# Optimization experiments

Hardware: AMD Instinct MI355X
Metric: run time of the kernel (lower is better)

## Reference

```python
import jax, jax.numpy as jnp
import numpy as np

B, S, E = 2, 2048, 2048
H, KV, D = 16, 4, 128


def setup_inputs() -> dict:
    key = jax.random.key(0)
    k0, k1, k2, k3, k4 = jax.random.split(key, 5)
    s = 0.02  # init scale for weights
    return {
        "x": jax.random.normal(k0, (B, S, E), jnp.float32),
        "wq": jax.random.normal(k1, (E, H * D), jnp.float32) * s,
        "wk": jax.random.normal(k2, (E, KV * D), jnp.float32) * s,
        "wv": jax.random.normal(k3, (E, KV * D), jnp.float32) * s,
        "wo": jax.random.normal(k4, (H * D, E), jnp.float32) * s,
    }


def _rope_tables(seq_len, head_dim, dtype):
    inv_freq = 1.0 / (10000.0 ** (jnp.arange(0, head_dim, 2, dtype=jnp.float32) / head_dim))
    t = jnp.arange(seq_len, dtype=jnp.float32)
    freqs = jnp.outer(t, inv_freq)  # [S, D/2]
    emb = jnp.concatenate([freqs, freqs], axis=-1)  # [S, D]
    cos = jnp.cos(emb).astype(dtype)[None, None]  # [1,1,S,D]
    sin = jnp.sin(emb).astype(dtype)[None, None]
    return cos, sin


def _rotate_half(x):
    x1, x2 = jnp.split(x, 2, axis=-1)
    return jnp.concatenate([-x2, x1], axis=-1)


def reference(x, wq, wk, wv, wo):
    b, s, _ = x.shape
    # projections -> [B, heads, S, D]
    q = (x @ wq).reshape(b, s, H, D).transpose(0, 2, 1, 3)
    k = (x @ wk).reshape(b, s, KV, D).transpose(0, 2, 1, 3)
    v = (x @ wv).reshape(b, s, KV, D).transpose(0, 2, 1, 3)
    # inline RoPE (rotate-half convention), applied to q and k
    cos, sin = _rope_tables(s, D, q.dtype)
    q = q * cos + _rotate_half(q) * sin
    k = k * cos + _rotate_half(k) * sin
    # GQA: duplicate K/V heads (repeat_interleave along head dim)
    rep = H // KV
    k = jnp.repeat(k, rep, axis=1)
    v = jnp.repeat(v, rep, axis=1)
    scale = 1.0 / np.sqrt(D)
    scores = jnp.einsum('bhqd,bhkd->bhqk', q, k) * scale  # [B,H,S,S]
    attn = jax.nn.softmax(scores.astype(jnp.float32), axis=-1).astype(q.dtype)
    out = jnp.einsum('bhqk,bhkd->bhqd', attn, v)  # [B,H,S,D]
    out = out.transpose(0, 2, 1, 3).reshape(b, s, H * D)
    return out @ wo
```

## Files before the change

kernel.cpp:

```cpp
#include <hip/hip_runtime.h>
#include <hip/hip_bf16.h>

typedef __attribute__((ext_vector_type(8))) short s16x8;
typedef __attribute__((ext_vector_type(4))) float f32x4;
typedef __attribute__((ext_vector_type(16))) float f32x16;

__device__ inline float bf2f(unsigned short u) {
  union { unsigned int i; float f; } v; v.i = ((unsigned int)u) << 16; return v.f;
}
__device__ inline unsigned short f2bf(float f) {
  union { float f; unsigned int i; } v; v.f = f;
  unsigned int r = (v.i + 0x7FFFu + ((v.i >> 16) & 1u)) >> 16;
  return (unsigned short)r;
}
__device__ inline void gl_lds16(const void* g, void* l) {
  __builtin_amdgcn_global_load_lds(
      (const __attribute__((address_space(1))) unsigned int*)g,
      (__attribute__((address_space(3))) unsigned int*)l, 16, 0, 0);
}

__global__ __launch_bounds__(256) void cast_to_bf16(const float* __restrict__ s,
                                                    unsigned short* __restrict__ d, int n4) {
  int i = blockIdx.x * 256 + threadIdx.x;
  if (i >= n4) return;
  float4 v = ((const float4*)s)[i];
  ushort4 o;
  o.x = f2bf(v.x); o.y = f2bf(v.y); o.z = f2bf(v.z); o.w = f2bf(v.w);
  ((ushort4*)d)[i] = o;
}

__global__ __launch_bounds__(256) void transpose_cast(const float* __restrict__ src,
                                                      unsigned short* __restrict__ dst,
                                                      int K, int N) {
  __shared__ float tile[32][33];
  int n0 = blockIdx.x * 32, k0 = blockIdx.y * 32;
  int tx = threadIdx.x & 31, ty = threadIdx.x >> 5;
#pragma unroll
  for (int i = 0; i < 4; ++i) {
    int k = ty + i * 8;
    tile[k][tx] = src[(size_t)(k0 + k) * N + n0 + tx];
  }
  __syncthreads();
#pragma unroll
  for (int i = 0; i < 4; ++i) {
    int n = ty + i * 8;
    dst[(size_t)(n0 + n) * K + k0 + tx] = f2bf(tile[tx][n]);
  }
}

__global__ __launch_bounds__(256) void rope_tables(float* __restrict__ ct, float* __restrict__ st) {
  int idx = blockIdx.x * 256 + threadIdx.x;
  int s = idx >> 6, i = idx & 63;
  float inv = powf(10000.0f, -(float)(2 * i) * (1.0f / 128.0f));
  float ang = (float)s * inv;
  ct[idx] = cosf(ang);
  st[idx] = sinf(ang);
}

__global__ __launch_bounds__(256) void rope_apply(unsigned short* __restrict__ qkv,
                                                  const float* __restrict__ ct,
                                                  const float* __restrict__ st) {
  int row = blockIdx.x;
  int pos = row & 2047;
  unsigned short* base = qkv + (size_t)row * 3072;
  for (int it = threadIdx.x; it < 1280; it += 256) {
    int head = it >> 6, dh = it & 63;
    int col = head < 16 ? head * 128 : 2048 + (head - 16) * 128;
    float a = bf2f(base[col + dh]);
    float b = bf2f(base[col + dh + 64]);
    float c = ct[pos * 64 + dh], sn = st[pos * 64 + dh];
    base[col + dh] = f2bf(a * c - b * sn);
    base[col + dh + 64] = f2bf(b * c + a * sn);
  }
}

__global__ __launch_bounds__(256) void vtrans(const unsigned short* __restrict__ qkv,
                                              unsigned short* __restrict__ vt) {
  __shared__ unsigned short tile[32][33];
  int tx = threadIdx.x & 31, ty = threadIdx.x >> 5;
  int s0 = blockIdx.x * 32;
  int d0 = blockIdx.y * 32;
  int bz = blockIdx.z;
  const unsigned short* src = qkv + (size_t)((bz >> 2) * 2048) * 3072 + 2560 + (bz & 3) * 128;
#pragma unroll
  for (int i = 0; i < 4; ++i)
    tile[ty + i * 8][tx] = src[(size_t)(s0 + ty + i * 8) * 3072 + d0 + tx];
  __syncthreads();
  unsigned short* dst = vt + (size_t)bz * 128 * 2048;
#pragma unroll
  for (int i = 0; i < 4; ++i)
    dst[(size_t)(d0 + ty + i * 8) * 2048 + s0 + tx] = tile[tx][ty + i * 8];
}

template <int BF16OUT>
__global__ __launch_bounds__(512, 2) void gemm256(const unsigned short* __restrict__ A,
                                                  const unsigned short* __restrict__ BT,
                                                  void* __restrict__ Cv,
                                                  int M, int N, int K) {
  __shared__ __align__(16) unsigned short Lds[2][4][256 * 32];
  const int t = threadIdx.x, lane = t & 63;
  const int wid = t >> 6, m16 = lane & 15, l4 = lane >> 4;
  const int wm = wid >> 2, wn = wid & 3;
  const int swA = (l4 ^ ((m16 >> 1) & 3)) * 16;

  int gx = gridDim.x, nwg = gx * gridDim.y;
  int wg = blockIdx.y * gx + blockIdx.x;
  if ((nwg & 7) == 0) { int q = nwg >> 3; wg = (wg & 7) * q + (wg >> 3); }
  const int rowBase = (wg / gx) * 256, colBase = (wg % gx) * 256;

  const int r0 = t >> 2, c80 = (t & 3) ^ ((r0 >> 1) & 3);
  const int g1 = 512 + t, r1 = g1 >> 2, c81 = (g1 & 3) ^ ((r1 >> 1) & 3);
  const char* pA0 = (const char*)(A + (size_t)(rowBase + r0) * K + c80 * 8);
  const char* pA1 = (const char*)(A + (size_t)(rowBase + r1) * K + c81 * 8);
  const char* pB0 = (const char*)(BT + (size_t)(colBase + r0) * K + c80 * 8);
  const char* pB1 = (const char*)(BT + (size_t)(colBase + r1) * K + c81 * 8);

  f32x4 acc[8][4];
#pragma unroll
  for (int fr = 0; fr < 8; ++fr)
#pragma unroll
    for (int fn = 0; fn < 4; ++fn) {
      f32x4 z = {0.f, 0.f, 0.f, 0.f};
      acc[fr][fn] = z;
    }
  s16x8 bf[4];

#define STG(mat, kc, kt, buf)                                             \
  {                                                                       \
    size_t ko = (size_t)((kt) * 64 + (kc) * 32) * 2;                      \
    char* pl = (char*)&Lds[buf][(mat) * 2 + (kc)][0];                     \
    gl_lds16(((mat) ? pB0 : pA0) + ko, pl + t * 16);                      \
    gl_lds16(((mat) ? pB1 : pA1) + ko, pl + 8192 + t * 16);               \
  }

#define GATE()                                         \
  asm volatile("s_waitcnt vmcnt(8)" ::: "memory");     \
  __builtin_amdgcn_s_barrier();                        \
  __builtin_amdgcn_sched_barrier(0);

#define CMP(cur, kc, frh)                                                          \
  {                                                                                \
    const char* Ap = (const char*)&Lds[cur][kc][0];                                \
    s16x8 af[4];                                                                   \
    _Pragma("unroll") for (int i = 0; i < 4; ++i)                                  \
        af[i] = *(const s16x8*)(Ap + (wm * 128 + ((frh) * 4 + i) * 16 + m16) * 64 + swA); \
    if ((frh) == 0) {                                                              \
      const char* Bp = (const char*)&Lds[cur][2 + (kc)][0];                        \
      _Pragma("unroll") for (int n = 0; n < 4; ++n)                                \
          bf[n] = *(const s16x8*)(Bp + (wn * 64 + n * 16 + m16) * 64 + swA);       \
    }                                                                              \
    __builtin_amdgcn_s_setprio(1);                                                 \
    _Pragma("unroll") for (int i = 0; i < 4; ++i)                                  \
        _Pragma("unroll") for (int n = 0; n < 4; ++n)                              \
            acc[(frh) * 4 + i][n] = __builtin_amdgcn_mfma_f32_16x16x32_bf16(       \
                af[i], bf[n], acc[(frh) * 4 + i][n], 0, 0, 0);                     \
    __builtin_amdgcn_s_setprio(0);                                                 \
  }

  const int NT = K >> 6;
  STG(0, 0, 0, 0); STG(1, 0, 0, 0);
  STG(0, 1, 0, 0); STG(1, 1, 0, 0);
  STG(0, 0, 1, 1); STG(1, 0, 1, 1);

  for (int kt = 0; kt < NT; ++kt) {
    const int cur = kt & 1;
    GATE();
    if (kt + 1 < NT) STG(0, 1, kt + 1, cur ^ 1);
    CMP(cur, 0, 0);
    __builtin_amdgcn_s_barrier();
    if (kt + 1 < NT) STG(1, 1, kt + 1, cur ^ 1);
    CMP(cur, 0, 1);
    GATE();
    if (kt + 2 < NT) STG(0, 0, kt + 2, cur);
    CMP(cur, 1, 0);
    __builtin_amdgcn_s_barrier();
    if (kt + 2 < NT) STG(1, 0, kt + 2, cur);
    CMP(cur, 1, 1);
  }
#undef STG
#undef GATE
#undef CMP

#pragma unroll
  for (int fr = 0; fr < 8; ++fr)
#pragma unroll
    for (int fn = 0; fn < 4; ++fn) {
      int rr = rowBase + wm * 128 + fr * 16 + l4 * 4;
      int cc = colBase + wn * 64 + fn * 16 + m16;
#pragma unroll
      for (int jr = 0; jr < 4; ++jr) {
        if (BF16OUT)
          ((unsigned short*)Cv)[(size_t)(rr + jr) * N + cc] = f2bf(acc[fr][fn][jr]);
        else
          ((float*)Cv)[(size_t)(rr + jr) * N + cc] = acc[fr][fn][jr];
      }
    }
}

__global__ __launch_bounds__(512, 2) void gemm256_n128(const unsigned short* __restrict__ A,
                                                       const unsigned short* __restrict__ BT,
                                                       float* __restrict__ Cv,
                                                       int M, int N, int K) {
  __shared__ __align__(16) char Lds[98304];
  const int t = threadIdx.x, lane = t & 63;
  const int wid = t >> 6, m16 = lane & 15, l4 = lane >> 4;
  const int wm = wid >> 2, wn = wid & 3;
  const int swA = (l4 ^ ((m16 >> 1) & 3)) * 16;

  int gx = gridDim.x, nwg = gx * gridDim.y;
  int wg = blockIdx.y * gx + blockIdx.x;
  if ((nwg & 7) == 0) { int q = nwg >> 3; wg = (wg & 7) * q + (wg >> 3); }
  const int rowBase = (wg / gx) * 256, colBase = (wg % gx) * 128;

  const int r0 = t >> 2, c80 = (t & 3) ^ ((r0 >> 1) & 3);
  const int g1 = 512 + t, r1 = g1 >> 2, c81 = (g1 & 3) ^ ((r1 >> 1) & 3);
  const char* pA0 = (const char*)(A + (size_t)(rowBase + r0) * K + c80 * 8);
  const char* pA1 = (const char*)(A + (size_t)(rowBase + r1) * K + c81 * 8);
  const char* pB0 = (const char*)(BT + (size_t)(colBase + r0) * K + c80 * 8);

  f32x4 acc[8][2];
#pragma unroll
  for (int fr = 0; fr < 8; ++fr)
#pragma unroll
    for (int fn = 0; fn < 2; ++fn) {
      f32x4 z = {0.f, 0.f, 0.f, 0.f};
      acc[fr][fn] = z;
    }
  s16x8 bf[2];

#define ABASE(buf, kc) (Lds + (buf) * 49152 + (kc) * 16384)
#define BBASE(buf, kc) (Lds + (buf) * 49152 + 32768 + (kc) * 8192)

#define STGA(kc, kt, buf)                                                 \
  {                                                                       \
    size_t ko = (size_t)((kt) * 64 + (kc) * 32) * 2;                      \
    gl_lds16(pA0 + ko, ABASE(buf, kc) + t * 16);                          \
    gl_lds16(pA1 + ko, ABASE(buf, kc) + 8192 + t * 16);                   \
  }
#define STGB(kc, kt, buf)                                                 \
  {                                                                       \
    size_t ko = (size_t)((kt) * 64 + (kc) * 32) * 2;                      \
    gl_lds16(pB0 + ko, BBASE(buf, kc) + t * 16);                          \
  }

#define GATE()                                         \
  asm volatile("s_waitcnt vmcnt(6)" ::: "memory");     \
  __builtin_amdgcn_s_barrier();                        \
  __builtin_amdgcn_sched_barrier(0);

#define CMP(cur, kc, frh)                                                          \
  {                                                                                \
    const char* Ap = ABASE(cur, kc);                                               \
    s16x8 af[4];                                                                   \
    _Pragma("unroll") for (int i = 0; i < 4; ++i)                                  \
        af[i] = *(const s16x8*)(Ap + (wm * 128 + ((frh) * 4 + i) * 16 + m16) * 64 + swA); \
    if ((frh) == 0) {                                                              \
      const char* Bp = BBASE(cur, kc);                                             \
      _Pragma("unroll") for (int n = 0; n < 2; ++n)                                \
          bf[n] = *(const s16x8*)(Bp + (wn * 32 + n * 16 + m16) * 64 + swA);       \
    }                                                                              \
    __builtin_amdgcn_s_setprio(1);                                                 \
    _Pragma("unroll") for (int i = 0; i < 4; ++i)                                  \
        _Pragma("unroll") for (int n = 0; n < 2; ++n)                              \
            acc[(frh) * 4 + i][n] = __builtin_amdgcn_mfma_f32_16x16x32_bf16(       \
                af[i], bf[n], acc[(frh) * 4 + i][n], 0, 0, 0);                     \
    __builtin_amdgcn_s_setprio(0);                                                 \
  }

  const int NT = K >> 6;
  STGA(0, 0, 0); STGB(0, 0, 0);
  STGA(1, 0, 0); STGB(1, 0, 0);
  STGA(0, 1, 1); STGB(0, 1, 1);

  for (int kt = 0; kt < NT; ++kt) {
    const int cur = kt & 1;
    GATE();
    if (kt + 1 < NT) STGA(1, kt + 1, cur ^ 1);
    CMP(cur, 0, 0);
    __builtin_amdgcn_s_barrier();
    if (kt + 1 < NT) STGB(1, kt + 1, cur ^ 1);
    CMP(cur, 0, 1);
    GATE();
    if (kt + 2 < NT) STGA(0, kt + 2, cur);
    CMP(cur, 1, 0);
    __builtin_amdgcn_s_barrier();
    if (kt + 2 < NT) STGB(0, kt + 2, cur);
    CMP(cur, 1, 1);
  }
#undef STGA
#undef STGB
#undef GATE
#undef CMP
#undef ABASE
#undef BBASE

#pragma unroll
  for (int fr = 0; fr < 8; ++fr)
#pragma unroll
    for (int fn = 0; fn < 2; ++fn) {
      int rr = rowBase + wm * 128 + fr * 16 + l4 * 4;
      int cc = colBase + wn * 32 + fn * 16 + m16;
#pragma unroll
      for (int jr = 0; jr < 4; ++jr)
        Cv[(size_t)(rr + jr) * N + cc] = acc[fr][fn][jr];
    }
}

__global__ __launch_bounds__(256, 2) void attn_kernel(const unsigned short* __restrict__ qkv,
                                                      const unsigned short* __restrict__ vt,
                                                      unsigned short* __restrict__ obuf) {
  __shared__ __align__(16) unsigned short Kl[2][64 * 128];
  __shared__ __align__(16) unsigned short Vl[2][128 * 64];
  const int t = threadIdx.x, lane = t & 63, w = t >> 6;
  const int q32 = lane & 31, l32 = lane >> 5;
  const int b = blockIdx.z, h = blockIdx.y, qb = blockIdx.x;
  const int kvh = h >> 2;
  const float SCL = 0.12751744616570824f;

  s16x8 qf[8];
  {
    const unsigned short* qp =
        qkv + (size_t)(b * 2048 + qb * 128 + w * 32 + q32) * 3072 + h * 128 + l32 * 8;
#pragma unroll
    for (int ds = 0; ds < 8; ++ds) qf[ds] = *(const s16x8*)(qp + ds * 16);
  }

  float lsum = 0.f;
  f32x16 acco[4];
#pragma unroll
  for (int dt = 0; dt < 4; ++dt) acco[dt] = (f32x16){};

  const char* pK[4];
  const char* pV[4];
#pragma unroll
  for (int i = 0; i < 4; ++i) {
    int c = i * 256 + t;
    {
      int row = c >> 4, ch = c & 15;
      pK[i] = (const char*)(qkv + (size_t)(b * 2048 + row) * 3072 + 2048 + kvh * 128) +
              ((ch * 16) ^ ((row & 7) << 4));
    }
    {
      int d = c >> 3, ch = c & 7;
      pV[i] = (const char*)(vt + (size_t)((b * 4 + kvh) * 128 + d) * 2048) +
              ((ch * 16) ^ ((d & 7) << 4));
    }
  }
  const size_t KADV = (size_t)64 * 3072 * 2;
  const size_t VADV = 128;

#define STAGE_T(buf)                                                         \
  {                                                                          \
    _Pragma("unroll") for (int i = 0; i < 4; ++i)                            \
        gl_lds16(pK[i], (char*)Kl[buf] + (i * 256 + t) * 16);                \
    _Pragma("unroll") for (int i = 0; i < 4; ++i)                            \
        gl_lds16(pV[i], (char*)Vl[buf] + (i * 256 + t) * 16);                \
    _Pragma("unroll") for (int i = 0; i < 4; ++i) pK[i] += KADV;             \
    _Pragma("unroll") for (int i = 0; i < 4; ++i) pV[i] += VADV;             \
  }

  int cur = 0;
  STAGE_T(0);

  for (int kt = 0; kt < 32; ++kt) {
    if (kt < 31) {
      STAGE_T(cur ^ 1);
      asm volatile("s_waitcnt vmcnt(8)" ::: "memory");
    } else {
      asm volatile("s_waitcnt vmcnt(0)" ::: "memory");
    }
    __builtin_amdgcn_s_barrier();
    __builtin_amdgcn_sched_barrier(0);

    f32x16 sc32[2];
    __builtin_amdgcn_s_setprio(1);
#pragma unroll
    for (int kt32 = 0; kt32 < 2; ++kt32) {
      f32x16 a = (f32x16){};
      int r = kt32 * 32 + q32;
      const char* kr = (const char*)Kl[cur] + r * 256;
      int sw = (r & 7) << 4;
#pragma unroll
      for (int ds = 0; ds < 8; ++ds) {
        s16x8 kf = *(const s16x8*)(kr + ((ds * 32 + l32 * 16) ^ sw));
        a = __builtin_amdgcn_mfma_f32_32x32x16_bf16(kf, qf[ds], a, 0, 0, 0);
      }
      sc32[kt32] = a;
    }
    __builtin_amdgcn_s_setprio(0);

    s16x8 bfrag[4];
    float part = 0.f;
#pragma unroll
    for (int kt32 = 0; kt32 < 2; ++kt32) {
      float e[16];
#pragma unroll
      for (int rg = 0; rg < 16; ++rg) {
        float x = sc32[kt32][rg] * SCL;
        asm("v_exp_f32 %0, %1" : "=v"(e[rg]) : "v"(x));
      }
#pragma unroll
      for (int rg = 0; rg < 16; ++rg) part += e[rg];
      unsigned int pr[4][2];
#pragma unroll
      for (int a2 = 0; a2 < 4; ++a2) {
        asm("v_cvt_pk_bf16_f32 %0, %1, %2"
            : "=v"(pr[a2][0]) : "v"(e[a2 * 4 + 0]), "v"(e[a2 * 4 + 1]));
        asm("v_cvt_pk_bf16_f32 %0, %1, %2"
            : "=v"(pr[a2][1]) : "v"(e[a2 * 4 + 2]), "v"(e[a2 * 4 + 3]));
      }
#pragma unroll
      for (int hf = 0; hf < 2; ++hf) {
        unsigned int x0 = pr[2 * hf][0], y0 = pr[2 * hf + 1][0];
        unsigned int x1 = pr[2 * hf][1], y1 = pr[2 * hf + 1][1];
        asm("v_permlane32_swap_b32 %0, %1" : "+v"(x0), "+v"(y0));
        asm("v_permlane32_swap_b32 %0, %1" : "+v"(x1), "+v"(y1));
        union { unsigned int u[4]; s16x8 v; } bb;
        bb.u[0] = x0; bb.u[1] = x1; bb.u[2] = y0; bb.u[3] = y1;
        bfrag[kt32 * 2 + hf] = bb.v;
      }
    }
    lsum += part;

    __builtin_amdgcn_s_setprio(1);
#pragma unroll
    for (int dt = 0; dt < 4; ++dt) {
      int d = dt * 32 + q32;
      const char* vr = (const char*)Vl[cur] + d * 128;
      int swv = (d & 7) << 4;
#pragma unroll
      for (int ts = 0; ts < 4; ++ts) {
        s16x8 vf = *(const s16x8*)(vr + ((ts * 32 + l32 * 16) ^ swv));
        acco[dt] = __builtin_amdgcn_mfma_f32_32x32x16_bf16(vf, bfrag[ts], acco[dt], 0, 0, 0);
      }
    }
    __builtin_amdgcn_s_setprio(0);
    __builtin_amdgcn_s_barrier();
    cur ^= 1;
  }
#undef STAGE_T

  {
    float s = lsum;
    s += __shfl_xor(s, 32);
    float iv = 1.0f / s;
    unsigned short* op =
        obuf + (size_t)(b * 2048 + qb * 128 + w * 32 + q32) * 2048 + h * 128;
#pragma unroll
    for (int dt = 0; dt < 4; ++dt)
#pragma unroll
      for (int rg = 0; rg < 16; ++rg) {
        int d = dt * 32 + (rg & 3) + 8 * (rg >> 2) + 4 * l32;
        op[d] = f2bf(acco[dt][rg] * iv);
      }
  }
}

extern "C" void kernel_launch(void* const* d_in, const int* in_sizes, int n_in,
                              void* d_out, int out_size, void* d_ws, size_t ws_size,
                              hipStream_t stream) {
  (void)in_sizes; (void)n_in; (void)out_size; (void)ws_size;
  const float* x  = (const float*)d_in[0];
  const float* wq = (const float*)d_in[1];
  const float* wk = (const float*)d_in[2];
  const float* wv = (const float*)d_in[3];
  const float* wo = (const float*)d_in[4];

  char* ws = (char*)d_ws;
  unsigned short* xb    = (unsigned short*)(ws);
  unsigned short* wqkvT = (unsigned short*)(ws + 16777216);
  unsigned short* woT   = (unsigned short*)(ws + 29360128);
  unsigned short* qkv   = (unsigned short*)(ws + 37748736);
  unsigned short* obuf  = (unsigned short*)(ws + 62914560);
  float* ct             = (float*)(ws + 79691776);
  float* st             = (float*)(ws + 80216064);
  unsigned short* vt    = xb;

  cast_to_bf16<<<8192, 256, 0, stream>>>(x, xb, 2097152);
  transpose_cast<<<dim3(64, 64), 256, 0, stream>>>(wq, wqkvT, 2048, 2048);
  transpose_cast<<<dim3(16, 64), 256, 0, stream>>>(wk, wqkvT + 2048 * 2048, 2048, 512);
  transpose_cast<<<dim3(16, 64), 256, 0, stream>>>(wv, wqkvT + 2560 * 2048, 2048, 512);
  transpose_cast<<<dim3(64, 64), 256, 0, stream>>>(wo, woT, 2048, 2048);
  rope_tables<<<512, 256, 0, stream>>>(ct, st);
  gemm256<1><<<dim3(12, 16), 512, 0, stream>>>(xb, wqkvT, qkv, 4096, 3072, 2048);
  rope_apply<<<4096, 256, 0, stream>>>(qkv, ct, st);
  vtrans<<<dim3(64, 4, 8), 256, 0, stream>>>(qkv, vt);
  attn_kernel<<<dim3(16, 16, 2), 256, 0, stream>>>(qkv, vt, obuf);
  gemm256_n128<<<dim3(16, 16), 512, 0, stream>>>(obuf, woT, (float*)d_out, 4096, 2048, 2048);
}
```

Baseline: 214.0 us.

## Process two 32-row query tiles per wave in attention kernel

Each wave now handles 64 query rows (two 32-row sub-tiles) instead of 32, so each K/V fragment read from LDS feeds two MFMAs. The grid is halved, and launch bounds drop to one block per SM to make room for the doubled accumulators and Q fragments. The aim is to halve K/V global and LDS traffic per query row. In exchange it adds register pressure, lowers occupancy, and leaves only 256 blocks over the device's CUs.

```diff
diff --git a/kernel.cpp b/kernel.cpp
--- a/kernel.cpp
+++ b/kernel.cpp
@@ -306,7 +306,7 @@
     }
 }
 
-__global__ __launch_bounds__(256, 2) void attn_kernel(const unsigned short* __restrict__ qkv,
+__global__ __launch_bounds__(256, 1) void attn_kernel(const unsigned short* __restrict__ qkv,
                                                       const unsigned short* __restrict__ vt,
                                                       unsigned short* __restrict__ obuf) {
   __shared__ __align__(16) unsigned short Kl[2][64 * 128];
@@ -317,18 +317,25 @@
   const int kvh = h >> 2;
   const float SCL = 0.12751744616570824f;
 
-  s16x8 qf[8];
+  s16x8 qf[2][8];
   {
     const unsigned short* qp =
-        qkv + (size_t)(b * 2048 + qb * 128 + w * 32 + q32) * 3072 + h * 128 + l32 * 8;
-#pragma unroll
-    for (int ds = 0; ds < 8; ++ds) qf[ds] = *(const s16x8*)(qp + ds * 16);
-  }
-
-  float lsum = 0.f;
-  f32x16 acco[4];
-#pragma unroll
-  for (int dt = 0; dt < 4; ++dt) acco[dt] = (f32x16){};
+        qkv + (size_t)(b * 2048 + qb * 256 + w * 64 + q32) * 3072 + h * 128 + l32 * 8;
+#pragma unroll
+    for (int qs = 0; qs < 2; ++qs)
+#pragma unroll
+      for (int ds = 0; ds < 8; ++ds)
+        qf[qs][ds] = *(const s16x8*)(qp + qs * 32 * 3072 + ds * 16);
+  }
+
+  float lsum[2];
+  f32x16 acco[2][4];
+#pragma unroll
+  for (int qs = 0; qs < 2; ++qs) {
+    lsum[qs] = 0.f;
+#pragma unroll
+    for (int dt = 0; dt < 4; ++dt) acco[qs][dt] = (f32x16){};
+  }
 
   const char* pK[4];
   const char* pV[4];
@@ -372,55 +379,61 @@
     __builtin_amdgcn_s_barrier();
     __builtin_amdgcn_sched_barrier(0);
 
-    f32x16 sc32[2];
+    f32x16 sc32[2][2];
     __builtin_amdgcn_s_setprio(1);
 #pragma unroll
     for (int kt32 = 0; kt32 < 2; ++kt32) {
-      f32x16 a = (f32x16){};
+      f32x16 a0 = (f32x16){};
+      f32x16 a1 = (f32x16){};
       int r = kt32 * 32 + q32;
       const char* kr = (const char*)Kl[cur] + r * 256;
       int sw = (r & 7) << 4;
 #pragma unroll
       for (int ds = 0; ds < 8; ++ds) {
         s16x8 kf = *(const s16x8*)(kr + ((ds * 32 + l32 * 16) ^ sw));
-        a = __builtin_amdgcn_mfma_f32_32x32x16_bf16(kf, qf[ds], a, 0, 0, 0);
+        a0 = __builtin_amdgcn_mfma_f32_32x32x16_bf16(kf, qf[0][ds], a0, 0, 0, 0);
+        a1 = __builtin_amdgcn_mfma_f32_32x32x16_bf16(kf, qf[1][ds], a1, 0, 0, 0);
       }
-      sc32[kt32] = a;
+      sc32[0][kt32] = a0;
+      sc32[1][kt32] = a1;
     }
     __builtin_amdgcn_s_setprio(0);
 
-    s16x8 bfrag[4];
-    float part = 0.f;
-#pragma unroll
-    for (int kt32 = 0; kt32 < 2; ++kt32) {
-      float e[16];
-#pragma unroll
-      for (int rg = 0; rg < 16; ++rg) {
-        float x = sc32[kt32][rg] * SCL;
-        asm("v_exp_f32 %0, %1" : "=v"(e[rg]) : "v"(x));
+    s16x8 bfrag[2][4];
+#pragma unroll
+    for (int qs = 0; qs < 2; ++qs) {
+      float part = 0.f;
+#pragma unroll
+      for (int kt32 = 0; kt32 < 2; ++kt32) {
+        float e[16];
+#pragma unroll
+        for (int rg = 0; rg < 16; ++rg) {
+          float x = sc32[qs][kt32][rg] * SCL;
+          asm("v_exp_f32 %0, %1" : "=v"(e[rg]) : "v"(x));
+        }
+#pragma unroll
+        for (int rg = 0; rg < 16; ++rg) part += e[rg];
+        unsigned int pr[4][2];
+#pragma unroll
+        for (int a2 = 0; a2 < 4; ++a2) {
+          asm("v_cvt_pk_bf16_f32 %0, %1, %2"
+              : "=v"(pr[a2][0]) : "v"(e[a2 * 4 + 0]), "v"(e[a2 * 4 + 1]));
+          asm("v_cvt_pk_bf16_f32 %0, %1, %2"
+              : "=v"(pr[a2][1]) : "v"(e[a2 * 4 + 2]), "v"(e[a2 * 4 + 3]));
+        }
+#pragma unroll
+        for (int hf = 0; hf < 2; ++hf) {
+          unsigned int x0 = pr[2 * hf][0], y0 = pr[2 * hf + 1][0];
+          unsigned int x1 = pr[2 * hf][1], y1 = pr[2 * hf + 1][1];
+          asm("v_permlane32_swap_b32 %0, %1" : "+v"(x0), "+v"(y0));
+          asm("v_permlane32_swap_b32 %0, %1" : "+v"(x1), "+v"(y1));
+          union { unsigned int u[4]; s16x8 v; } bb;
+          bb.u[0] = x0; bb.u[1] = x1; bb.u[2] = y0; bb.u[3] = y1;
+          bfrag[qs][kt32 * 2 + hf] = bb.v;
+        }
       }
-#pragma unroll
-      for (int rg = 0; rg < 16; ++rg) part += e[rg];
-      unsigned int pr[4][2];
-#pragma unroll
-      for (int a2 = 0; a2 < 4; ++a2) {
-        asm("v_cvt_pk_bf16_f32 %0, %1, %2"
-            : "=v"(pr[a2][0]) : "v"(e[a2 * 4 + 0]), "v"(e[a2 * 4 + 1]));
-        asm("v_cvt_pk_bf16_f32 %0, %1, %2"
-            : "=v"(pr[a2][1]) : "v"(e[a2 * 4 + 2]), "v"(e[a2 * 4 + 3]));
-      }
-#pragma unroll
-      for (int hf = 0; hf < 2; ++hf) {
-        unsigned int x0 = pr[2 * hf][0], y0 = pr[2 * hf + 1][0];
-        unsigned int x1 = pr[2 * hf][1], y1 = pr[2 * hf + 1][1];
-        asm("v_permlane32_swap_b32 %0, %1" : "+v"(x0), "+v"(y0));
-        asm("v_permlane32_swap_b32 %0, %1" : "+v"(x1), "+v"(y1));
-        union { unsigned int u[4]; s16x8 v; } bb;
-        bb.u[0] = x0; bb.u[1] = x1; bb.u[2] = y0; bb.u[3] = y1;
-        bfrag[kt32 * 2 + hf] = bb.v;
-      }
-    }
-    lsum += part;
+      lsum[qs] += part;
+    }
 
     __builtin_amdgcn_s_setprio(1);
 #pragma unroll
@@ -431,7 +444,8 @@
 #pragma unroll
       for (int ts = 0; ts < 4; ++ts) {
         s16x8 vf = *(const s16x8*)(vr + ((ts * 32 + l32 * 16) ^ swv));
-        acco[dt] = __builtin_amdgcn_mfma_f32_32x32x16_bf16(vf, bfrag[ts], acco[dt], 0, 0, 0);
+        acco[0][dt] = __builtin_amdgcn_mfma_f32_32x32x16_bf16(vf, bfrag[0][ts], acco[0][dt], 0, 0, 0);
+        acco[1][dt] = __builtin_amdgcn_mfma_f32_32x32x16_bf16(vf, bfrag[1][ts], acco[1][dt], 0, 0, 0);
       }
     }
     __builtin_amdgcn_s_setprio(0);
@@ -440,18 +454,19 @@
   }
 #undef STAGE_T
 
-  {
-    float s = lsum;
+#pragma unroll
+  for (int qs = 0; qs < 2; ++qs) {
+    float s = lsum[qs];
     s += __shfl_xor(s, 32);
     float iv = 1.0f / s;
     unsigned short* op =
-        obuf + (size_t)(b * 2048 + qb * 128 + w * 32 + q32) * 2048 + h * 128;
+        obuf + (size_t)(b * 2048 + qb * 256 + w * 64 + qs * 32 + q32) * 2048 + h * 128;
 #pragma unroll
     for (int dt = 0; dt < 4; ++dt)
 #pragma unroll
       for (int rg = 0; rg < 16; ++rg) {
         int d = dt * 32 + (rg & 3) + 8 * (rg >> 2) + 4 * l32;
-        op[d] = f2bf(acco[dt][rg] * iv);
+        op[d] = f2bf(acco[qs][dt][rg] * iv);
       }
   }
 }
@@ -485,6 +500,6 @@
   gemm256<1><<<dim3(12, 16), 512, 0, stream>>>(xb, wqkvT, qkv, 4096, 3072, 2048);
   rope_apply<<<4096, 256, 0, stream>>>(qkv, ct, st);
   vtrans<<<dim3(64, 4, 8), 256, 0, stream>>>(qkv, vt);
-  attn_kernel<<<dim3(16, 16, 2), 256, 0, stream>>>(qkv, vt, obuf);
+  attn_kernel<<<dim3(8, 16, 2), 256, 0, stream>>>(qkv, vt, obuf);
   gemm256_n128<<<dim3(16, 16), 512, 0, stream>>>(obuf, woT, (float*)d_out, 4096, 2048, 2048);
 }
```

After: 230.4 us. 7.6% more time.
